# Performance work log

Measured on AMD Instinct MI355X. Metric: run time of the kernel, lower is better.

## Reference

```python
import jax, jax.numpy as jnp
import numpy as np

B, N, K, M, FD = 8, 2048, 20, 2025, 512


def knn_idx(x, k):
    # x: (B,N,C). pairwise_distance = -||xi||^2 + 2 xi.xj - ||xj||^2; topk of that = k nearest (self included)
    xx = jnp.sum(x * x, axis=-1)  # (B,N)
    neg_d = 2.0 * jnp.einsum('bnc,bmc->bnm', x, x) - xx[:, :, None] - xx[:, None, :]
    return jax.lax.top_k(neg_d, k)[1]  # (B,N,k) int32


def edge_conv(x, w, s, b, k=K):
    # EdgeConv block: knn gather -> cat(nb - x, x) -> 1x1 conv (no bias) -> BN(eval, mean 0 var 1) -> LeakyReLU(0.2) -> max over k
    idx = knn_idx(x, k)
    nb = jax.vmap(lambda f, i: f[i])(x, idx)            # (B,N,k,C)
    ctr = jnp.broadcast_to(x[:, :, None, :], nb.shape)
    feat = jnp.concatenate([nb - ctr, ctr], axis=-1)    # (B,N,k,2C)
    h = jnp.einsum('bnkc,oc->bnko', feat, w)
    h = jax.nn.leaky_relu(h * s + b, 0.2)
    return jnp.max(h, axis=2)                           # (B,N,O)


def mlp3(h, w1, b1, w2, b2, w3, b3):
    # folding MLP: three 1x1 Conv1d layers with ReLU between
    h = jax.nn.relu(jnp.einsum('bmc,oc->bmo', h, w1) + b1)
    h = jax.nn.relu(jnp.einsum('bmc,oc->bmo', h, w2) + b2)
    return jnp.einsum('bmc,oc->bmo', h, w3) + b3


def build_grid():
    g = jnp.linspace(-0.3, 0.3, 45)
    # itertools.product(x, y): first coord varies slowest -> meshgrid indexing='ij'
    return jnp.stack(jnp.meshgrid(g, g, indexing='ij'), axis=-1).reshape(M, 2)


def setup_inputs() -> dict:
    key = jax.random.key(0)
    ks = iter(jax.random.split(key, 40))
    d = {'points': jax.random.normal(next(ks), (B, N, 3), jnp.float32)}
    def w(shape):
        return jax.random.normal(next(ks), shape, jnp.float32) * 0.05
    def sc(shape):
        return jax.random.uniform(next(ks), shape, jnp.float32, 0.5, 1.5)
    d['w1'], d['s1'], d['b1'] = w((64, 6)), sc((64,)), w((64,))
    d['w2'], d['s2'], d['b2'] = w((64, 128)), sc((64,)), w((64,))
    d['w3'], d['s3'], d['b3'] = w((128, 128)), sc((128,)), w((128,))
    d['w4'], d['s4'], d['b4'] = w((256, 256)), sc((256,)), w((256,))
    d['w5'], d['s5'], d['b5'] = w((FD, 512)), sc((FD,)), w((FD,))
    d['f1w1'], d['f1b1'] = w((FD, FD + 2)), w((FD,))
    d['f1w2'], d['f1b2'] = w((FD, FD)), w((FD,))
    d['f1w3'], d['f1b3'] = w((3, FD)), w((3,))
    d['f2w1'], d['f2b1'] = w((FD, FD + 3)), w((FD,))
    d['f2w2'], d['f2b2'] = w((FD, FD)), w((FD,))
    d['f2w3'], d['f2b3'] = w((3, FD)), w((3,))
    return d


def reference(points, w1, s1, b1, w2, s2, b2, w3, s3, b3, w4, s4, b4, w5, s5, b5,
              f1w1, f1b1, f1w2, f1b2, f1w3, f1b3, f2w1, f2b1, f2w2, f2b2, f2w3, f2b3):
    # ---- DGCNN_Cls_Encoder ----
    x1 = edge_conv(points, w1, s1, b1)   # (B,N,64)
    x2 = edge_conv(x1, w2, s2, b2)       # (B,N,64)
    x3 = edge_conv(x2, w3, s3, b3)       # (B,N,128)
    x4 = edge_conv(x3, w4, s4, b4)       # (B,N,256)
    xc = jnp.concatenate([x1, x2, x3, x4], axis=-1)            # (B,N,512)
    x0 = jax.nn.leaky_relu(jnp.einsum('bnc,oc->bno', xc, w5) * s5 + b5, 0.2)
    feat = jnp.max(x0, axis=1)                                  # (B,FD) global codeword
    # ---- FoldNet_Decoder (plane) ----
    xr = jnp.broadcast_to(feat[:, None, :], (feat.shape[0], M, FD))
    grid = jnp.broadcast_to(build_grid()[None], (feat.shape[0], M, 2))
    fr1 = mlp3(jnp.concatenate([xr, grid], axis=-1), f1w1, f1b1, f1w2, f1b2, f1w3, f1b3)
    fr2 = mlp3(jnp.concatenate([xr, fr1], axis=-1), f2w1, f2b1, f2w2, f2b2, f2w3, f2b3)
    return fr2                                                   # (B,2025,3)
```

## Files before the change

### kernel.cpp

```cpp
#include <hip/hip_runtime.h>
#include <cstddef>
#include <cstdint>

#define LRELU(v) ((v) > 0.f ? (v) : 0.2f*(v))

constexpr int Bb = 8, Nn = 2048, Kk = 20, Mm = 2025, FD = 512;
constexpr int CMCH = 32;

__global__ __launch_bounds__(256)
void rownorm_kernel(const float* __restrict__ x, int ldx, int C,
                    float* __restrict__ norms, int rows) {
  int row = blockIdx.x * 4 + (threadIdx.x >> 6);
  int lane = threadIdx.x & 63;
  if (row >= rows) return;
  const float* xr = x + (size_t)row * ldx;
  float s = 0.f;
  for (int c = lane; c < C; c += 64) { float v = xr[c]; s += v * v; }
  for (int off = 32; off; off >>= 1) s += __shfl_xor(s, off);
  if (lane == 0) norms[row] = s;
}

__global__ __launch_bounds__(256)
void dist_kernel(const float* __restrict__ x, int ldx, int C,
                 const float* __restrict__ norms,
                 float* __restrict__ dist,
                 long long xstride, long long dstride, int nstride) {
  int bz = blockIdx.z;
  x     += (size_t)bz * xstride;
  norms += (size_t)bz * nstride;
  dist  += (size_t)bz * dstride;

  __shared__ float As[32][36];
  __shared__ float Bs[32][36];
  int t  = threadIdx.x;
  int tx = t & 31, ty = t >> 5;
  int row0 = blockIdx.y * 32, col0 = blockIdx.x * 32;
  float acc[4] = {0.f, 0.f, 0.f, 0.f};

  for (int cc = 0; cc < C; cc += 32) {
    int gk = cc + tx;
    bool kok = gk < C;
#pragma unroll
    for (int i = 0; i < 4; i++) {
      int r = ty + 8 * i;
      As[tx][r] = kok ? x[(size_t)(row0 + r) * ldx + gk] : 0.f;
      Bs[tx][r] = kok ? x[(size_t)(col0 + r) * ldx + gk] : 0.f;
    }
    __syncthreads();
#pragma unroll
    for (int k = 0; k < 32; k++) {
      float bv = Bs[k][tx];
      float4 a = *(const float4*)&As[k][ty * 4];
      acc[0] += a.x * bv; acc[1] += a.y * bv;
      acc[2] += a.z * bv; acc[3] += a.w * bv;
    }
    __syncthreads();
  }
#pragma unroll
  for (int i = 0; i < 4; i++) {
    int n_ = row0 + ty * 4 + i;
    int m_ = col0 + tx;
    dist[(size_t)n_ * Nn + m_] = 2.f * acc[i] - norms[n_] - norms[m_];
  }
}

__global__ __launch_bounds__(256)
void topk20_kernel(const float* __restrict__ dist, int* __restrict__ idx,
                   long long dstride) {
  int bz = blockIdx.z;
  dist += (size_t)bz * dstride;
  idx  += (size_t)bz * Nn * Kk;
  int row  = blockIdx.x * 4 + (threadIdx.x >> 6);
  int lane = threadIdx.x & 63;
  const float* dr = dist + (size_t)row * Nn;
  float v[32];
#pragma unroll
  for (int j = 0; j < 32; j++) v[j] = dr[lane + 64 * j];
  unsigned taken = 0u;
  for (int t = 0; t < Kk; t++) {
    float best = -3.4e38f; int bj = 40;
#pragma unroll
    for (int j = 0; j < 32; j++) {
      if (!(taken & (1u << j)) && v[j] > best) { best = v[j]; bj = j; }
    }
    int bm = lane + (bj << 6);
    for (int off = 32; off; off >>= 1) {
      float ob = __shfl_xor(best, off);
      int   om = __shfl_xor(bm, off);
      if (ob > best || (ob == best && om < bm)) { best = ob; bm = om; }
    }
    if (lane == 0) idx[row * Kk + t] = bm;
    if ((bm & 63) == lane) taken |= 1u << (bm >> 6);
  }
}

__device__ inline void prep_w_dev(const float* __restrict__ w, float* __restrict__ wA,
                                  float* __restrict__ wD, int t, int C) {
  int o = t / C, c = t % C;
  float a = w[(size_t)o * 2 * C + c];
  float b = w[(size_t)o * 2 * C + C + c];
  wA[t] = a;
  wD[t] = b - a;
}

__global__ void prep_all_kernel(const float* __restrict__ w1, const float* __restrict__ w2,
                                const float* __restrict__ w3, const float* __restrict__ w4,
                                const float* __restrict__ f1w1, const float* __restrict__ f2w1,
                                float* wA1, float* wD1, float* wA2, float* wD2,
                                float* wA3, float* wD3, float* wA4, float* wD4,
                                float* wt1, float* wt2, float* grid) {
  int t = blockIdx.x * 256 + threadIdx.x;
  if (t < 192) {
    prep_w_dev(w1, wA1, wD1, t, 3);
  } else if (t < 4288) {
    prep_w_dev(w2, wA2, wD2, t - 192, 64);
  } else if (t < 12480) {
    prep_w_dev(w3, wA3, wD3, t - 4288, 64);
  } else if (t < 45248) {
    prep_w_dev(w4, wA4, wD4, t - 12480, 128);
  } else if (t < 46272) {
    int local = t - 45248;
    int c = local / FD, o = local % FD;
    wt1[c * FD + o] = f1w1[(size_t)o * (FD + 2) + FD + c];
  } else if (t < 47808) {
    int local = t - 46272;
    int c = local / FD, o = local % FD;
    wt2[c * FD + o] = f2w1[(size_t)o * (FD + 3) + FD + c];
  } else if (t < 49833) {
    int m = t - 47808;
    int i = m / 45, j = m % 45;
    const double step = 0.6 / 44.0;
    grid[m * 2 + 0] = (float)(-0.3 + step * i);
    grid[m * 2 + 1] = (float)(-0.3 + step * j);
  }
}

template <int EPI>
__global__ __launch_bounds__(256)
void gemm_kernel(const float* __restrict__ A, int lda,
                 const float* __restrict__ Bw, int ldb,
                 const float* __restrict__ scale, const float* __restrict__ bias,
                 float* __restrict__ out, int ldo,
                 int M, int Ncols, int K) {
  __shared__ float As[16][68];
  __shared__ float Bs[16][68];
  int t  = threadIdx.x;
  int lk = t & 15, lm = t >> 4;
  int tx = t & 15, ty = t >> 4;
  int row0 = blockIdx.x * 64, col0 = blockIdx.y * 64;
  float acc[4][4] = {{0.f}};

  for (int kc = 0; kc < K; kc += 16) {
    int gk = kc + lk;
    bool kok = gk < K;
#pragma unroll
    for (int i = 0; i < 4; i++) {
      int m  = lm + 16 * i;
      int gr = row0 + m;
      int gc = col0 + m;
      As[lk][m] = (kok && gr < M)     ? A[(size_t)gr * lda + gk]  : 0.f;
      Bs[lk][m] = (kok && gc < Ncols) ? Bw[(size_t)gc * ldb + gk] : 0.f;
    }
    __syncthreads();
#pragma unroll
    for (int k = 0; k < 16; k++) {
      float4 a = *(const float4*)&As[k][ty * 4];
      float4 b = *(const float4*)&Bs[k][tx * 4];
      acc[0][0] += a.x * b.x; acc[0][1] += a.x * b.y; acc[0][2] += a.x * b.z; acc[0][3] += a.x * b.w;
      acc[1][0] += a.y * b.x; acc[1][1] += a.y * b.y; acc[1][2] += a.y * b.z; acc[1][3] += a.y * b.w;
      acc[2][0] += a.z * b.x; acc[2][1] += a.z * b.y; acc[2][2] += a.z * b.z; acc[2][3] += a.z * b.w;
      acc[3][0] += a.w * b.x; acc[3][1] += a.w * b.y; acc[3][2] += a.w * b.z; acc[3][3] += a.w * b.w;
    }
    __syncthreads();
  }

  float sv[4] = {0.f,0.f,0.f,0.f}, bv[4] = {0.f,0.f,0.f,0.f};
#pragma unroll
  for (int j = 0; j < 4; j++) {
    int c = col0 + tx * 4 + j;
    if constexpr (EPI == 1) { sv[j] = scale[c]; bv[j] = bias[c]; }
    else if constexpr (EPI == 2 || EPI == 3) { bv[j] = bias[c]; }
  }
#pragma unroll
  for (int i = 0; i < 4; i++) {
    int gr = row0 + ty * 4 + i;
    if (gr >= M) continue;
    float r[4];
#pragma unroll
    for (int j = 0; j < 4; j++) {
      float v = acc[i][j];
      if constexpr (EPI == 1) { v = v * sv[j] + bv[j]; v = LRELU(v); }
      else if constexpr (EPI == 2) { v = fmaxf(v + bv[j], 0.f); }
      else if constexpr (EPI == 3) { v = v + bv[j]; }
      r[j] = v;
    }
    *(float4*)&out[(size_t)gr * ldo + col0 + tx * 4] = make_float4(r[0], r[1], r[2], r[3]);
  }
}

template <int EPI>
__global__ __launch_bounds__(256)
void gemm_big_kernel(const float* __restrict__ A, int lda, long long astride,
                     const float* __restrict__ Bw, int ldb, long long bstride,
                     const float* __restrict__ rn, const float* __restrict__ cn,
                     int nstride,
                     const float* __restrict__ scale, const float* __restrict__ bias,
                     float* __restrict__ out, int ldo, long long ostride,
                     int M, int K) {
  int bz = blockIdx.z;
  A   += (size_t)bz * astride;
  Bw  += (size_t)bz * bstride;
  out += (size_t)bz * ostride;
  if constexpr (EPI == 4) { rn += (size_t)bz * nstride; cn += (size_t)bz * nstride; }

  __shared__ float As[32][132];
  __shared__ float Bs[32][132];
  int t  = threadIdx.x;
  int tx = t & 15, ty = t >> 4;
  int row0 = blockIdx.x * 128, col0 = blockIdx.y * 128;

  int lr = t >> 3;
  int lk = (t & 7) * 4;

  float acc[8][8] = {{0.f}};

  for (int kc = 0; kc < K; kc += 32) {
#pragma unroll
    for (int g = 0; g < 4; g++) {
      int r  = lr + 32 * g;
      int gr = row0 + r;
      float4 av = make_float4(0.f, 0.f, 0.f, 0.f);
      if (gr < M) av = *(const float4*)&A[(size_t)gr * lda + kc + lk];
      float4 bv = *(const float4*)&Bw[(size_t)(col0 + r) * ldb + kc + lk];
      As[lk + 0][r] = av.x; As[lk + 1][r] = av.y; As[lk + 2][r] = av.z; As[lk + 3][r] = av.w;
      Bs[lk + 0][r] = bv.x; Bs[lk + 1][r] = bv.y; Bs[lk + 2][r] = bv.z; Bs[lk + 3][r] = bv.w;
    }
    __syncthreads();
#pragma unroll
    for (int k = 0; k < 32; k++) {
      float4 a0 = *(const float4*)&As[k][ty * 4];
      float4 a1 = *(const float4*)&As[k][64 + ty * 4];
      float4 b0 = *(const float4*)&Bs[k][tx * 4];
      float4 b1 = *(const float4*)&Bs[k][64 + tx * 4];
      float a[8] = {a0.x, a0.y, a0.z, a0.w, a1.x, a1.y, a1.z, a1.w};
      float b[8] = {b0.x, b0.y, b0.z, b0.w, b1.x, b1.y, b1.z, b1.w};
#pragma unroll
      for (int i = 0; i < 8; i++)
#pragma unroll
        for (int j = 0; j < 8; j++)
          acc[i][j] += a[i] * b[j];
    }
    __syncthreads();
  }

  int gcol[8];
  float sv[8], bv2[8], cnv[8];
#pragma unroll
  for (int j = 0; j < 8; j++) {
    int c = (j < 4) ? (tx * 4 + j) : (64 + tx * 4 + (j - 4));
    gcol[j] = col0 + c;
    if constexpr (EPI == 1) { sv[j] = scale[gcol[j]]; bv2[j] = bias[gcol[j]]; }
    if constexpr (EPI == 2) { bv2[j] = bias[gcol[j]]; }
    if constexpr (EPI == 4) { cnv[j] = cn[gcol[j]]; }
  }
#pragma unroll
  for (int i = 0; i < 8; i++) {
    int r  = (i < 4) ? (ty * 4 + i) : (64 + ty * 4 + (i - 4));
    int gr = row0 + r;
    if (gr >= M) continue;
    float rni = 0.f;
    if constexpr (EPI == 4) rni = rn[gr];
    float res[8];
#pragma unroll
    for (int j = 0; j < 8; j++) {
      float v = acc[i][j];
      if constexpr (EPI == 1) { v = v * sv[j] + bv2[j]; v = LRELU(v); }
      else if constexpr (EPI == 2) { v = fmaxf(v + bv2[j], 0.f); }
      else if constexpr (EPI == 4) { v = 2.f * v - rni - cnv[j]; }
      res[j] = v;
    }
    *(float4*)&out[(size_t)gr * ldo + gcol[0]] = make_float4(res[0], res[1], res[2], res[3]);
    *(float4*)&out[(size_t)gr * ldo + gcol[4]] = make_float4(res[4], res[5], res[6], res[7]);
  }
}

template <int EPI>
__global__ __launch_bounds__(256)
void gemm_med_kernel(const float* __restrict__ A, int lda,
                     const float* __restrict__ Bw, int ldb,
                     const float* __restrict__ scale, const float* __restrict__ bias,
                     float* __restrict__ out, int ldo,
                     int M, int K) {
  __shared__ float As[32][132];
  __shared__ float Bs[32][68];
  int t  = threadIdx.x;
  int tx = t & 15, ty = t >> 4;
  int row0 = blockIdx.x * 128, col0 = blockIdx.y * 64;

  int lr = t >> 3;
  int lk = (t & 7) * 4;

  float acc[8][4] = {{0.f}};

  for (int kc = 0; kc < K; kc += 32) {
#pragma unroll
    for (int g = 0; g < 4; g++) {
      int r  = lr + 32 * g;
      int gr = row0 + r;
      float4 av = make_float4(0.f, 0.f, 0.f, 0.f);
      if (gr < M) av = *(const float4*)&A[(size_t)gr * lda + kc + lk];
      As[lk + 0][r] = av.x; As[lk + 1][r] = av.y; As[lk + 2][r] = av.z; As[lk + 3][r] = av.w;
    }
#pragma unroll
    for (int g = 0; g < 2; g++) {
      int r = lr + 32 * g;
      float4 bv = *(const float4*)&Bw[(size_t)(col0 + r) * ldb + kc + lk];
      Bs[lk + 0][r] = bv.x; Bs[lk + 1][r] = bv.y; Bs[lk + 2][r] = bv.z; Bs[lk + 3][r] = bv.w;
    }
    __syncthreads();
#pragma unroll
    for (int k = 0; k < 32; k++) {
      float4 a0 = *(const float4*)&As[k][ty * 4];
      float4 a1 = *(const float4*)&As[k][64 + ty * 4];
      float4 b0 = *(const float4*)&Bs[k][tx * 4];
      float a[8] = {a0.x, a0.y, a0.z, a0.w, a1.x, a1.y, a1.z, a1.w};
      float b[4] = {b0.x, b0.y, b0.z, b0.w};
#pragma unroll
      for (int i = 0; i < 8; i++)
#pragma unroll
        for (int j = 0; j < 4; j++)
          acc[i][j] += a[i] * b[j];
    }
    __syncthreads();
  }

  int gcol[4];
  float sv[4], bv2[4];
#pragma unroll
  for (int j = 0; j < 4; j++) {
    gcol[j] = col0 + tx * 4 + j;
    if constexpr (EPI == 1) { sv[j] = scale[gcol[j]]; bv2[j] = bias[gcol[j]]; }
    if constexpr (EPI == 2) { bv2[j] = bias[gcol[j]]; }
  }
#pragma unroll
  for (int i = 0; i < 8; i++) {
    int r  = (i < 4) ? (ty * 4 + i) : (64 + ty * 4 + (i - 4));
    int gr = row0 + r;
    if (gr >= M) continue;
    float res[4];
#pragma unroll
    for (int j = 0; j < 4; j++) {
      float v = acc[i][j];
      if constexpr (EPI == 1) { v = v * sv[j] + bv2[j]; v = LRELU(v); }
      else if constexpr (EPI == 2) { v = fmaxf(v + bv2[j], 0.f); }
      res[j] = v;
    }
    *(float4*)&out[(size_t)gr * ldo + gcol[0]] = make_float4(res[0], res[1], res[2], res[3]);
  }
}

__global__ void gather_max_kernel(const float* __restrict__ PQ,
                                  const int* __restrict__ idx,
                                  const float* __restrict__ s, const float* __restrict__ bi,
                                  float* __restrict__ out, int ldo, int O) {
  int n = blockIdx.x;
  int o = threadIdx.x;
  int b = n >> 11;
  int ld2 = 2 * O;
  __shared__ int sidx[Kk];
  if (o < Kk) sidx[o] = idx[(size_t)n * Kk + o];
  __syncthreads();
  float q = PQ[(size_t)n * ld2 + O + o];
  float sc = s[o], bb = bi[o];
  float m = -3.4e38f;
#pragma unroll
  for (int k = 0; k < Kk; k++) {
    int mm = sidx[k];
    float h = (PQ[((size_t)(b * Nn + mm)) * ld2 + o] + q) * sc + bb;
    h = LRELU(h);
    m = fmaxf(m, h);
  }
  out[(size_t)n * ldo + o] = m;
}

__global__ __launch_bounds__(256)
void colmax_part_kernel(const float* __restrict__ x0, float* __restrict__ part) {
  int b = blockIdx.x;
  int o = blockIdx.y * 256 + threadIdx.x;
  int ch = blockIdx.z;
  const int ROWS = Nn / CMCH;
  const float* p = x0 + ((size_t)b * Nn + (size_t)ch * ROWS) * FD + o;
  float m = -3.4e38f;
  for (int n = 0; n < ROWS; n++) m = fmaxf(m, p[(size_t)n * FD]);
  part[((size_t)b * CMCH + ch) * FD + o] = m;
}

__global__ __launch_bounds__(256)
void colmax_final_kernel(const float* __restrict__ part, float* __restrict__ feat) {
  int b = blockIdx.x;
  int o = blockIdx.y * 256 + threadIdx.x;
  const float* p = part + (size_t)b * CMCH * FD + o;
  float m = -3.4e38f;
  for (int c = 0; c < CMCH; c++) m = fmaxf(m, p[(size_t)c * FD]);
  feat[b * FD + o] = m;
}

__global__ __launch_bounds__(512)
void fold_l1_kernel(const float* __restrict__ fb, const float* __restrict__ extra,
                    int ec, int emod, const float* __restrict__ wt,
                    float* __restrict__ out) {
  int r = blockIdx.x;
  int o = threadIdx.x;
  int b = r / Mm;
  int er = emod ? (r % emod) : r;
  float v = fb[b * FD + o];
  for (int c = 0; c < ec; c++) v += extra[(size_t)er * ec + c] * wt[c * FD + o];
  out[(size_t)r * FD + o] = fmaxf(v, 0.f);
}

__global__ __launch_bounds__(256)
void gemm_o3_kernel(const float* __restrict__ A, const float* __restrict__ W,
                    const float* __restrict__ bias, float* __restrict__ out, int M) {
  int r = blockIdx.x * 4 + (threadIdx.x >> 6);
  int lane = threadIdx.x & 63;
  if (r >= M) return;
  const float* ar = A + (size_t)r * FD;
  float a0 = 0.f, a1 = 0.f, a2 = 0.f;
  for (int c = lane; c < FD; c += 64) {
    float av = ar[c];
    a0 += av * W[c];
    a1 += av * W[FD + c];
    a2 += av * W[2 * FD + c];
  }
  for (int off = 32; off; off >>= 1) {
    a0 += __shfl_xor(a0, off);
    a1 += __shfl_xor(a1, off);
    a2 += __shfl_xor(a2, off);
  }
  if (lane == 0) {
    out[r * 3 + 0] = a0 + bias[0];
    out[r * 3 + 1] = a1 + bias[1];
    out[r * 3 + 2] = a2 + bias[2];
  }
}

extern "C" void kernel_launch(void* const* d_in, const int* in_sizes, int n_in,
                              void* d_out, int out_size, void* d_ws, size_t ws_size,
                              hipStream_t stream) {
  const float* points = (const float*)d_in[0];
  const float* w1 = (const float*)d_in[1],  *s1 = (const float*)d_in[2],  *b1 = (const float*)d_in[3];
  const float* w2 = (const float*)d_in[4],  *s2 = (const float*)d_in[5],  *b2 = (const float*)d_in[6];
  const float* w3 = (const float*)d_in[7],  *s3 = (const float*)d_in[8],  *b3 = (const float*)d_in[9];
  const float* w4 = (const float*)d_in[10], *s4 = (const float*)d_in[11], *b4 = (const float*)d_in[12];
  const float* w5 = (const float*)d_in[13], *s5 = (const float*)d_in[14], *b5 = (const float*)d_in[15];
  const float* f1w1 = (const float*)d_in[16], *f1b1 = (const float*)d_in[17];
  const float* f1w2 = (const float*)d_in[18], *f1b2 = (const float*)d_in[19];
  const float* f1w3 = (const float*)d_in[20], *f1b3 = (const float*)d_in[21];
  const float* f2w1 = (const float*)d_in[22], *f2b1 = (const float*)d_in[23];
  const float* f2w2 = (const float*)d_in[24], *f2b2 = (const float*)d_in[25];
  const float* f2w3 = (const float*)d_in[26], *f2b3 = (const float*)d_in[27];

  float* ws = (float*)d_ws;
  size_t off = 0;
  auto alloc = [&](size_t n) { float* p = ws + off; off += (n + 63) & ~(size_t)63; return p; };

  const int BN = Bb * Nn;
  float* p_feat = alloc(Bb * FD);
  float* p_fr1  = alloc(Bb * Mm * 3);
  float* p_norm = alloc(BN);
  int*   p_idx  = (int*)alloc((size_t)BN * Kk);
  float* p_wA1  = alloc(64 * 3);    float* p_wD1 = alloc(64 * 3);
  float* p_wA2  = alloc(64 * 64);   float* p_wD2 = alloc(64 * 64);
  float* p_wA3  = alloc(128 * 64);  float* p_wD3 = alloc(128 * 64);
  float* p_wA4  = alloc(256 * 128); float* p_wD4 = alloc(256 * 128);
  float* p_grid = alloc(Mm * 2);
  float* p_wt1  = alloc(2 * FD);
  float* p_wt2  = alloc(3 * FD);
  float* p_fb   = alloc(Bb * FD);
  float* p_part = alloc((size_t)Bb * CMCH * FD);
  float* p_xc   = alloc((size_t)BN * FD);
  float* p_PQ   = alloc((size_t)BN * 512);
  float* p_H    = alloc((size_t)BN * FD);
  float* p_H2   = p_xc;

  size_t distN = (size_t)Nn * Nn;
  bool bigws = ws_size >= (off + (size_t)Bb * distN) * sizeof(float);
  float* p_dist = bigws ? (ws + off) : p_PQ;

  prep_all_kernel<<<195, 256, 0, stream>>>(w1, w2, w3, w4, f1w1, f2w1,
                                           p_wA1, p_wD1, p_wA2, p_wD2,
                                           p_wA3, p_wD3, p_wA4, p_wD4,
                                           p_wt1, p_wt2, p_grid);

  auto edgeconv = [&](const float* x, int ldx, int C, int O,
                      const float* wA,
                      const float* sc, const float* bb,
                      float* outp, int ldo) {
    rownorm_kernel<<<BN / 4, 256, 0, stream>>>(x, ldx, C, p_norm, BN);
    if (C == 3) {
      if (bigws) {
        dist_kernel<<<dim3(64, 64, Bb), 256, 0, stream>>>(
            x, ldx, C, p_norm, p_dist, (long long)Nn * ldx, (long long)distN, Nn);
        topk20_kernel<<<dim3(Nn / 4, 1, Bb), 256, 0, stream>>>(p_dist, p_idx, (long long)distN);
      } else {
        for (int b = 0; b < Bb; b++) {
          dist_kernel<<<dim3(64, 64, 1), 256, 0, stream>>>(
              x + (size_t)b * Nn * ldx, ldx, C, p_norm + b * Nn, p_dist, 0, 0, 0);
          topk20_kernel<<<dim3(Nn / 4, 1, 1), 256, 0, stream>>>(
              p_dist, p_idx + (size_t)b * Nn * Kk, 0);
        }
      }
    } else {
      if (bigws) {
        gemm_big_kernel<4><<<dim3(16, 16, Bb), 256, 0, stream>>>(
            x, ldx, (long long)Nn * ldx, x, ldx, (long long)Nn * ldx,
            p_norm, p_norm, Nn, nullptr, nullptr,
            p_dist, Nn, (long long)distN, Nn, C);
        topk20_kernel<<<dim3(Nn / 4, 1, Bb), 256, 0, stream>>>(p_dist, p_idx, (long long)distN);
      } else {
        for (int b = 0; b < Bb; b++) {
          gemm_big_kernel<4><<<dim3(16, 16, 1), 256, 0, stream>>>(
              x + (size_t)b * Nn * ldx, ldx, 0, x + (size_t)b * Nn * ldx, ldx, 0,
              p_norm + b * Nn, p_norm + b * Nn, 0, nullptr, nullptr,
              p_dist, Nn, 0, Nn, C);
          topk20_kernel<<<dim3(Nn / 4, 1, 1), 256, 0, stream>>>(
              p_dist, p_idx + (size_t)b * Nn * Kk, 0);
        }
      }
    }
    int N2 = 2 * O;
    if (C % 32 == 0) {
      gemm_med_kernel<0><<<dim3(BN / 128, N2 / 64), 256, 0, stream>>>(
          x, ldx, wA, C, nullptr, nullptr, p_PQ, N2, BN, C);
    } else {
      gemm_kernel<0><<<dim3(BN / 64, N2 / 64), 256, 0, stream>>>(
          x, ldx, wA, C, nullptr, nullptr, p_PQ, N2, BN, N2, C);
    }
    gather_max_kernel<<<BN, O, 0, stream>>>(p_PQ, p_idx, sc, bb, outp, ldo, O);
  };

  edgeconv(points,     3,  3,   64,  p_wA1, s1, b1, p_xc + 0,   FD);
  edgeconv(p_xc + 0,   FD, 64,  64,  p_wA2, s2, b2, p_xc + 64,  FD);
  edgeconv(p_xc + 64,  FD, 64,  128, p_wA3, s3, b3, p_xc + 128, FD);
  edgeconv(p_xc + 128, FD, 128, 256, p_wA4, s4, b4, p_xc + 256, FD);

  gemm_med_kernel<1><<<dim3(BN / 128, FD / 64), 256, 0, stream>>>(
      p_xc, FD, w5, FD, s5, b5, p_H, FD, BN, FD);
  colmax_part_kernel<<<dim3(Bb, FD / 256, CMCH), 256, 0, stream>>>(p_H, p_part);
  colmax_final_kernel<<<dim3(Bb, FD / 256), 256, 0, stream>>>(p_part, p_feat);

  const int MD = Bb * Mm;
  const int GX = (MD + 127) / 128;
  gemm_kernel<3><<<dim3(1, FD / 64), 256, 0, stream>>>(
      p_feat, FD, f1w1, FD + 2, nullptr, f1b1, p_fb, FD, Bb, FD, FD);
  fold_l1_kernel<<<MD, FD, 0, stream>>>(p_fb, p_grid, 2, Mm, p_wt1, p_H);
  gemm_med_kernel<2><<<dim3(GX, FD / 64), 256, 0, stream>>>(
      p_H, FD, f1w2, FD, nullptr, f1b2, p_H2, FD, MD, FD);
  gemm_o3_kernel<<<(MD + 3) / 4, 256, 0, stream>>>(p_H2, f1w3, f1b3, p_fr1, MD);

  gemm_kernel<3><<<dim3(1, FD / 64), 256, 0, stream>>>(
      p_feat, FD, f2w1, FD + 3, nullptr, f2b1, p_fb, FD, Bb, FD, FD);
  fold_l1_kernel<<<MD, FD, 0, stream>>>(p_fb, p_fr1, 3, 0, p_wt2, p_H);
  gemm_med_kernel<2><<<dim3(GX, FD / 64), 256, 0, stream>>>(
      p_H, FD, f2w2, FD, nullptr, f2b2, p_H2, FD, MD, FD);
  gemm_o3_kernel<<<(MD + 3) / 4, 256, 0, stream>>>(p_H2, f2w3, f2b3, (float*)d_out, MD);
}
```

Baseline: 1.539 ms.

## Run 512-wide GEMMs on bf16 MFMA with three-way split precision emulation

Adds a split3 kernel that breaks fp32 operands into three bf16 planes, and an MFMA-based 128x128 GEMM that accumulates six cross products to approximate fp32 accuracy. The conv5 layer and both folding second layers use it in place of the scalar FP32 tiled GEMM, and the now-unused epilogue paths are removed from the old kernels. The aim is to move the dominant dense GEMM FLOPs onto matrix cores, at the cost of extra passes that split activations and weights and more memory traffic from the three planes.

```diff
diff --git a/kernel.cpp b/kernel.cpp
--- a/kernel.cpp
+++ b/kernel.cpp
@@ -6,6 +6,118 @@
 
 constexpr int Bb = 8, Nn = 2048, Kk = 20, Mm = 2025, FD = 512;
 constexpr int CMCH = 32;
+
+typedef __attribute__((ext_vector_type(8))) short short8v;
+typedef __attribute__((ext_vector_type(4))) float f32x4;
+
+__device__ inline unsigned short f2bf(float x) {
+  unsigned int u = __float_as_uint(x);
+  u += 0x7fff + ((u >> 16) & 1);
+  return (unsigned short)(u >> 16);
+}
+__device__ inline float bf2f(unsigned short h) {
+  return __uint_as_float(((unsigned int)h) << 16);
+}
+
+__global__ __launch_bounds__(256)
+void split3_kernel(const float* __restrict__ x, unsigned short* __restrict__ o,
+                   long long plane, int n) {
+  for (int i = blockIdx.x * 256 + threadIdx.x; i < n; i += gridDim.x * 256) {
+    float v = x[i];
+    unsigned short h1 = f2bf(v);
+    float r1 = v - bf2f(h1);
+    unsigned short h2 = f2bf(r1);
+    unsigned short h3 = f2bf(r1 - bf2f(h2));
+    o[i] = h1;
+    o[plane + i] = h2;
+    o[2 * plane + i] = h3;
+  }
+}
+
+template <int EPI>
+__global__ __launch_bounds__(256, 2)
+void gemm_mfma512_kernel(const unsigned short* __restrict__ A3, long long aplane,
+                         const unsigned short* __restrict__ B3, long long bplane,
+                         const float* __restrict__ scale, const float* __restrict__ bias,
+                         float* __restrict__ out, int M) {
+  constexpr int LDT = 40;
+  __shared__ unsigned short As[3][128 * LDT];
+  __shared__ unsigned short Bs[3][128 * LDT];
+  int t = threadIdx.x;
+  int w = t >> 6, l = t & 63;
+  int wr = w >> 1, wc = w & 1;
+  int lr = l & 15, lg = l >> 4;
+  int row0 = blockIdx.x * 128, col0 = blockIdx.y * 128;
+
+  f32x4 acc[4][4];
+#pragma unroll
+  for (int m = 0; m < 4; m++)
+#pragma unroll
+    for (int n = 0; n < 4; n++) acc[m][n] = (f32x4){0.f, 0.f, 0.f, 0.f};
+
+  for (int kc = 0; kc < 512; kc += 32) {
+#pragma unroll
+    for (int p = 0; p < 3; p++) {
+#pragma unroll
+      for (int r = 0; r < 2; r++) {
+        int flat = r * 256 + t;
+        int ar = flat >> 2, seg = flat & 3;
+        int ka = kc + seg * 8;
+        uint4 av = make_uint4(0u, 0u, 0u, 0u);
+        int gr = row0 + ar;
+        if (gr < M) av = *(const uint4*)&A3[(size_t)p * aplane + (size_t)gr * 512 + ka];
+        *(uint4*)&As[p][ar * LDT + seg * 8] = av;
+        uint4 bv = *(const uint4*)&B3[(size_t)p * bplane + (size_t)(col0 + ar) * 512 + ka];
+        *(uint4*)&Bs[p][ar * LDT + seg * 8] = bv;
+      }
+    }
+    __syncthreads();
+
+    short8v afr[3][4];
+#pragma unroll
+    for (int p = 0; p < 3; p++)
+#pragma unroll
+      for (int m = 0; m < 4; m++)
+        afr[p][m] = *(const short8v*)&As[p][(wr * 64 + m * 16 + lr) * LDT + lg * 8];
+#pragma unroll
+    for (int n = 0; n < 4; n++) {
+      int bo = (wc * 64 + n * 16 + lr) * LDT + lg * 8;
+      short8v b0 = *(const short8v*)&Bs[0][bo];
+      short8v b1 = *(const short8v*)&Bs[1][bo];
+      short8v b2 = *(const short8v*)&Bs[2][bo];
+#pragma unroll
+      for (int m = 0; m < 4; m++) {
+        acc[m][n] = __builtin_amdgcn_mfma_f32_16x16x32_bf16(afr[0][m], b0, acc[m][n], 0, 0, 0);
+        acc[m][n] = __builtin_amdgcn_mfma_f32_16x16x32_bf16(afr[0][m], b1, acc[m][n], 0, 0, 0);
+        acc[m][n] = __builtin_amdgcn_mfma_f32_16x16x32_bf16(afr[1][m], b0, acc[m][n], 0, 0, 0);
+        acc[m][n] = __builtin_amdgcn_mfma_f32_16x16x32_bf16(afr[0][m], b2, acc[m][n], 0, 0, 0);
+        acc[m][n] = __builtin_amdgcn_mfma_f32_16x16x32_bf16(afr[1][m], b1, acc[m][n], 0, 0, 0);
+        acc[m][n] = __builtin_amdgcn_mfma_f32_16x16x32_bf16(afr[2][m], b0, acc[m][n], 0, 0, 0);
+      }
+    }
+    __syncthreads();
+  }
+
+#pragma unroll
+  for (int n = 0; n < 4; n++) {
+    int col = col0 + wc * 64 + n * 16 + lr;
+    float sv = 0.f, bvv = 0.f;
+    if constexpr (EPI == 1) { sv = scale[col]; bvv = bias[col]; }
+    if constexpr (EPI == 2) { bvv = bias[col]; }
+#pragma unroll
+    for (int m = 0; m < 4; m++) {
+#pragma unroll
+      for (int j = 0; j < 4; j++) {
+        int gr = row0 + wr * 64 + m * 16 + lg * 4 + j;
+        if (gr >= M) continue;
+        float v = acc[m][n][j];
+        if constexpr (EPI == 1) { v = v * sv + bvv; v = LRELU(v); }
+        if constexpr (EPI == 2) { v = fmaxf(v + bvv, 0.f); }
+        out[(size_t)gr * 512 + col] = v;
+      }
+    }
+  }
+}
 
 __global__ __launch_bounds__(256)
 void rownorm_kernel(const float* __restrict__ x, int ldx, int C,
@@ -174,12 +286,11 @@
     __syncthreads();
   }
 
-  float sv[4] = {0.f,0.f,0.f,0.f}, bv[4] = {0.f,0.f,0.f,0.f};
+  float bv[4] = {0.f,0.f,0.f,0.f};
 #pragma unroll
   for (int j = 0; j < 4; j++) {
     int c = col0 + tx * 4 + j;
-    if constexpr (EPI == 1) { sv[j] = scale[c]; bv[j] = bias[c]; }
-    else if constexpr (EPI == 2 || EPI == 3) { bv[j] = bias[c]; }
+    if constexpr (EPI == 3) { bv[j] = bias[c]; }
   }
 #pragma unroll
   for (int i = 0; i < 4; i++) {
@@ -189,9 +300,7 @@
 #pragma unroll
     for (int j = 0; j < 4; j++) {
       float v = acc[i][j];
-      if constexpr (EPI == 1) { v = v * sv[j] + bv[j]; v = LRELU(v); }
-      else if constexpr (EPI == 2) { v = fmaxf(v + bv[j], 0.f); }
-      else if constexpr (EPI == 3) { v = v + bv[j]; }
+      if constexpr (EPI == 3) { v = v + bv[j]; }
       r[j] = v;
     }
     *(float4*)&out[(size_t)gr * ldo + col0 + tx * 4] = make_float4(r[0], r[1], r[2], r[3]);
@@ -254,13 +363,11 @@
   }
 
   int gcol[8];
-  float sv[8], bv2[8], cnv[8];
+  float cnv[8];
 #pragma unroll
   for (int j = 0; j < 8; j++) {
     int c = (j < 4) ? (tx * 4 + j) : (64 + tx * 4 + (j - 4));
     gcol[j] = col0 + c;
-    if constexpr (EPI == 1) { sv[j] = scale[gcol[j]]; bv2[j] = bias[gcol[j]]; }
-    if constexpr (EPI == 2) { bv2[j] = bias[gcol[j]]; }
     if constexpr (EPI == 4) { cnv[j] = cn[gcol[j]]; }
   }
 #pragma unroll
@@ -274,9 +381,7 @@
 #pragma unroll
     for (int j = 0; j < 8; j++) {
       float v = acc[i][j];
-      if constexpr (EPI == 1) { v = v * sv[j] + bv2[j]; v = LRELU(v); }
-      else if constexpr (EPI == 2) { v = fmaxf(v + bv2[j], 0.f); }
-      else if constexpr (EPI == 4) { v = 2.f * v - rni - cnv[j]; }
+      if constexpr (EPI == 4) { v = 2.f * v - rni - cnv[j]; }
       res[j] = v;
     }
     *(float4*)&out[(size_t)gr * ldo + gcol[0]] = make_float4(res[0], res[1], res[2], res[3]);
@@ -334,28 +439,13 @@
     __syncthreads();
   }
 
-  int gcol[4];
-  float sv[4], bv2[4];
-#pragma unroll
-  for (int j = 0; j < 4; j++) {
-    gcol[j] = col0 + tx * 4 + j;
-    if constexpr (EPI == 1) { sv[j] = scale[gcol[j]]; bv2[j] = bias[gcol[j]]; }
-    if constexpr (EPI == 2) { bv2[j] = bias[gcol[j]]; }
-  }
 #pragma unroll
   for (int i = 0; i < 8; i++) {
     int r  = (i < 4) ? (ty * 4 + i) : (64 + ty * 4 + (i - 4));
     int gr = row0 + r;
     if (gr >= M) continue;
-    float res[4];
-#pragma unroll
-    for (int j = 0; j < 4; j++) {
-      float v = acc[i][j];
-      if constexpr (EPI == 1) { v = v * sv[j] + bv2[j]; v = LRELU(v); }
-      else if constexpr (EPI == 2) { v = fmaxf(v + bv2[j], 0.f); }
-      res[j] = v;
-    }
-    *(float4*)&out[(size_t)gr * ldo + gcol[0]] = make_float4(res[0], res[1], res[2], res[3]);
+    *(float4*)&out[(size_t)gr * ldo + col0 + tx * 4] =
+        make_float4(acc[i][0], acc[i][1], acc[i][2], acc[i][3]);
   }
 }
 
@@ -465,6 +555,8 @@
   auto alloc = [&](size_t n) { float* p = ws + off; off += (n + 63) & ~(size_t)63; return p; };
 
   const int BN = Bb * Nn;
+  const long long WPL = 262144;
+  const long long APL = (long long)BN * FD;
   float* p_feat = alloc(Bb * FD);
   float* p_fr1  = alloc(Bb * Mm * 3);
   float* p_norm = alloc(BN);
@@ -478,6 +570,10 @@
   float* p_wt2  = alloc(3 * FD);
   float* p_fb   = alloc(Bb * FD);
   float* p_part = alloc((size_t)Bb * CMCH * FD);
+  unsigned short* p_w5s   = (unsigned short*)alloc(3 * WPL / 2);
+  unsigned short* p_f1w2s = (unsigned short*)alloc(3 * WPL / 2);
+  unsigned short* p_f2w2s = (unsigned short*)alloc(3 * WPL / 2);
+  unsigned short* p_As    = (unsigned short*)alloc(3 * (size_t)APL / 2);
   float* p_xc   = alloc((size_t)BN * FD);
   float* p_PQ   = alloc((size_t)BN * 512);
   float* p_H    = alloc((size_t)BN * FD);
@@ -491,10 +587,12 @@
                                            p_wA1, p_wD1, p_wA2, p_wD2,
                                            p_wA3, p_wD3, p_wA4, p_wD4,
                                            p_wt1, p_wt2, p_grid);
+  split3_kernel<<<512, 256, 0, stream>>>(w5,   p_w5s,   WPL, (int)WPL);
+  split3_kernel<<<512, 256, 0, stream>>>(f1w2, p_f1w2s, WPL, (int)WPL);
+  split3_kernel<<<512, 256, 0, stream>>>(f2w2, p_f2w2s, WPL, (int)WPL);
 
   auto edgeconv = [&](const float* x, int ldx, int C, int O,
-                      const float* wA,
-                      const float* sc, const float* bb,
+                      const float* wA, const float* sc, const float* bb,
                       float* outp, int ldo) {
     rownorm_kernel<<<BN / 4, 256, 0, stream>>>(x, ldx, C, p_norm, BN);
     if (C == 3) {
@@ -544,24 +642,27 @@
   edgeconv(p_xc + 64,  FD, 64,  128, p_wA3, s3, b3, p_xc + 128, FD);
   edgeconv(p_xc + 128, FD, 128, 256, p_wA4, s4, b4, p_xc + 256, FD);
 
-  gemm_med_kernel<1><<<dim3(BN / 128, FD / 64), 256, 0, stream>>>(
-      p_xc, FD, w5, FD, s5, b5, p_H, FD, BN, FD);
+  split3_kernel<<<2048, 256, 0, stream>>>(p_xc, p_As, APL, BN * FD);
+  gemm_mfma512_kernel<1><<<dim3(BN / 128, 4), 256, 0, stream>>>(
+      p_As, APL, p_w5s, WPL, s5, b5, p_H, BN);
   colmax_part_kernel<<<dim3(Bb, FD / 256, CMCH), 256, 0, stream>>>(p_H, p_part);
   colmax_final_kernel<<<dim3(Bb, FD / 256), 256, 0, stream>>>(p_part, p_feat);
 
   const int MD = Bb * Mm;
-  const int GX = (MD + 127) / 128;
+  const int GXM = (MD + 127) / 128;
   gemm_kernel<3><<<dim3(1, FD / 64), 256, 0, stream>>>(
       p_feat, FD, f1w1, FD + 2, nullptr, f1b1, p_fb, FD, Bb, FD, FD);
   fold_l1_kernel<<<MD, FD, 0, stream>>>(p_fb, p_grid, 2, Mm, p_wt1, p_H);
-  gemm_med_kernel<2><<<dim3(GX, FD / 64), 256, 0, stream>>>(
-      p_H, FD, f1w2, FD, nullptr, f1b2, p_H2, FD, MD, FD);
+  split3_kernel<<<2048, 256, 0, stream>>>(p_H, p_As, APL, MD * FD);
+  gemm_mfma512_kernel<2><<<dim3(GXM, 4), 256, 0, stream>>>(
+      p_As, APL, p_f1w2s, WPL, nullptr, f1b2, p_H2, MD);
   gemm_o3_kernel<<<(MD + 3) / 4, 256, 0, stream>>>(p_H2, f1w3, f1b3, p_fr1, MD);
 
   gemm_kernel<3><<<dim3(1, FD / 64), 256, 0, stream>>>(
       p_feat, FD, f2w1, FD + 3, nullptr, f2b1, p_fb, FD, Bb, FD, FD);
   fold_l1_kernel<<<MD, FD, 0, stream>>>(p_fb, p_fr1, 3, 0, p_wt2, p_H);
-  gemm_med_kernel<2><<<dim3(GX, FD / 64), 256, 0, stream>>>(
-      p_H, FD, f2w2, FD, nullptr, f2b2, p_H2, FD, MD, FD);
+  split3_kernel<<<2048, 256, 0, stream>>>(p_H, p_As, APL, MD * FD);
+  gemm_mfma512_kernel<2><<<dim3(GXM, 4), 256, 0, stream>>>(
+      p_As, APL, p_f2w2s, WPL, nullptr, f2b2, p_H2, MD);
   gemm_o3_kernel<<<(MD + 3) / 4, 256, 0, stream>>>(p_H2, f2w3, f2b3, (float*)d_out, MD);
 }
```

Measured after the change: 2.267 ms. 1.47x slower.
